# Kernel tuning notes

Measured on AMD Instinct MI355X. Metric: run time of the kernel, lower is better.

## Reference

```python
import jax, jax.numpy as jnp
import numpy as np

B, S, D, H, DFF = 2, 2048, 1024, 16, 4096
DK = D // H
EPS = 1e-5


def layer_norm(x, gamma, beta, eps=EPS):
    mu = jnp.mean(x, axis=-1, keepdims=True)
    var = jnp.mean(jnp.square(x - mu), axis=-1, keepdims=True)
    return (x - mu) * jax.lax.rsqrt(var + eps) * gamma + beta


def setup_inputs() -> dict:
    key = jax.random.key(0)
    ks = jax.random.split(key, 12)
    s_d = 1.0 / np.sqrt(D)
    s_f = 1.0 / np.sqrt(DFF)
    return {
        "x": jax.random.normal(ks[0], (B, S, D), jnp.float32),
        # per-head QKV projections stacked: [H, D, DK]
        "Wq": jax.random.normal(ks[1], (H, D, DK), jnp.float32) * s_d,
        "bq": jnp.zeros((H, DK), jnp.float32),
        "Wk": jax.random.normal(ks[2], (H, D, DK), jnp.float32) * s_d,
        "bk": jnp.zeros((H, DK), jnp.float32),
        "Wv": jax.random.normal(ks[3], (H, D, DK), jnp.float32) * s_d,
        "bv": jnp.zeros((H, DK), jnp.float32),
        "Wo": jax.random.normal(ks[4], (D, D), jnp.float32) * s_d,
        "bo": jnp.zeros((D,), jnp.float32),
        "W1": jax.random.normal(ks[5], (D, DFF), jnp.float32) * s_d,
        "b1": jnp.zeros((DFF,), jnp.float32),
        "W2": jax.random.normal(ks[6], (DFF, D), jnp.float32) * s_f,
        "b2": jnp.zeros((D,), jnp.float32),
        "ln1_g": jnp.ones((D,), jnp.float32),
        "ln1_b": jnp.zeros((D,), jnp.float32),
        "ln2_g": jnp.ones((D,), jnp.float32),
        "ln2_b": jnp.zeros((D,), jnp.float32),
    }


def reference(x, Wq, bq, Wk, bk, Wv, bv, Wo, bo, W1, b1, W2, b2,
              ln1_g, ln1_b, ln2_g, ln2_b):
    # --- residual 1: pre-norm multi-head self-attention (mask unused, dropout=eval) ---
    h = layer_norm(x, ln1_g, ln1_b)                      # [B,S,D]
    q = jnp.einsum('bsd,hdk->bhsk', h, Wq) + bq[:, None, :]
    k = jnp.einsum('bsd,hdk->bhsk', h, Wk) + bk[:, None, :]
    v = jnp.einsum('bsd,hdk->bhsk', h, Wv) + bv[:, None, :]
    scores = jnp.einsum('bhsk,bhtk->bhst', q, k) / np.sqrt(DK)  # [B,H,S,S]
    w = jax.nn.softmax(scores, axis=-1)
    ctx = jnp.einsum('bhst,bhtk->bhsk', w, v)            # [B,H,S,DK]
    # concat heads along feature dim -> [B,S,D]
    ctx = jnp.transpose(ctx, (0, 2, 1, 3)).reshape(B, S, D)
    attn_out = ctx @ Wo + bo
    x = x + attn_out
    # --- residual 2: pre-norm feed-forward ---
    h2 = layer_norm(x, ln2_g, ln2_b)
    ff = jax.nn.relu(h2 @ W1 + b1) @ W2 + b2
    return x + ff
```

## Files before the change

### kernel.cpp

```cpp
#include <hip/hip_runtime.h>

#define B_   2
#define S_   2048
#define D_   1024
#define H_   16
#define DK_  64
#define DFF_ 4096
#define NT_  (B_*S_)
#define QS_  3072

using u16 = unsigned short;
typedef __attribute__((ext_vector_type(8))) short bf16x8;
typedef __attribute__((ext_vector_type(4))) float f32x4;
typedef __attribute__((ext_vector_type(4))) u16  u16x4;

__device__ __forceinline__ float bf2f(u16 h) {
  union { unsigned u; float f; } c; c.u = ((unsigned)h) << 16; return c.f;
}
__device__ __forceinline__ u16 f2bf(float f) {
  union { float f; unsigned u; } c; c.f = f;
  unsigned u = c.u;
  return (u16)((u + 0x7fffu + ((u >> 16) & 1u)) >> 16);
}
__device__ __forceinline__ u16 f2bf_up(float f) {
  union { float f; unsigned u; } c; c.f = f;
  return (u16)((c.u + 0x8000u) >> 16);
}

__device__ __forceinline__ void load_lds16(const void* g, void* l) {
  __builtin_amdgcn_global_load_lds(
      (const __attribute__((address_space(1))) unsigned int*)g,
      (__attribute__((address_space(3))) unsigned int*)l, 16, 0, 0);
}

__device__ __forceinline__ void store_out(u16* p, float v)   { *p = f2bf(v); }
__device__ __forceinline__ void store_out(float* p, float v) { *p = v; }

__global__ __launch_bounds__(256) void ln_kernel(
    const float* __restrict__ x, const float* __restrict__ g,
    const float* __restrict__ bt, u16* __restrict__ o)
{
  const int row = blockIdx.x, t = threadIdx.x;
  const float4 xv = *(const float4*)(x + (size_t)row * D_ + t * 4);
  float f[4] = {xv.x, xv.y, xv.z, xv.w};
  float sum = f[0] + f[1] + f[2] + f[3];
  float sq  = f[0]*f[0] + f[1]*f[1] + f[2]*f[2] + f[3]*f[3];
#pragma unroll
  for (int d = 32; d >= 1; d >>= 1) {
    sum += __shfl_down(sum, d);
    sq  += __shfl_down(sq, d);
  }
  __shared__ float red[8];
  const int lane = t & 63, wid = t >> 6;
  if (lane == 0) { red[wid] = sum; red[wid + 4] = sq; }
  __syncthreads();
  sum = red[0] + red[1] + red[2] + red[3];
  sq  = red[4] + red[5] + red[6] + red[7];
  const float mu   = sum * (1.0f / D_);
  const float var  = sq * (1.0f / D_) - mu * mu;
  const float rstd = rsqrtf(var + 1e-5f);
  const float4 gv = *(const float4*)(g  + t * 4);
  const float4 bv = *(const float4*)(bt + t * 4);
  u16x4 ov;
  ov[0] = f2bf((f[0] - mu) * rstd * gv.x + bv.x);
  ov[1] = f2bf((f[1] - mu) * rstd * gv.y + bv.y);
  ov[2] = f2bf((f[2] - mu) * rstd * gv.z + bv.z);
  ov[3] = f2bf((f[3] - mu) * rstd * gv.w + bv.w);
  *(u16x4*)(o + (size_t)row * D_ + t * 4) = ov;
}

__global__ __launch_bounds__(256) void transpose_h(
    const float* __restrict__ in, u16* __restrict__ out, int R, int C)
{
  __shared__ float tile[32][33];
  const int z = blockIdx.z;
  const float* ip = in  + (size_t)z * R * C;
  u16*         op = out + (size_t)z * R * C;
  const int c0 = blockIdx.x * 32, r0 = blockIdx.y * 32;
  const int tx = threadIdx.x & 31, ty = threadIdx.x >> 5;
#pragma unroll
  for (int i = 0; i < 32; i += 8)
    tile[ty + i][tx] = ip[(size_t)(r0 + ty + i) * C + c0 + tx];
  __syncthreads();
#pragma unroll
  for (int i = 0; i < 32; i += 8)
    op[(size_t)(c0 + ty + i) * R + r0 + tx] = f2bf(tile[tx][ty + i]);
}

__global__ __launch_bounds__(256) void transpose_qkv(
    const float* __restrict__ Wq, const float* __restrict__ Wk,
    const float* __restrict__ Wv, u16* __restrict__ out)
{
  __shared__ float tile[32][33];
  const int z = blockIdx.z;
  const int which = z >> 4, h = z & 15;
  const float* ip = (which == 0 ? Wq : which == 1 ? Wk : Wv) + (size_t)h * 1024 * 64;
  u16* op = out + ((size_t)which * 1024 + h * 64) * 1024;
  const float sc = (which == 0) ? 0.125f : 1.0f;
  const int c0 = blockIdx.x * 32, r0 = blockIdx.y * 32;
  const int tx = threadIdx.x & 31, ty = threadIdx.x >> 5;
#pragma unroll
  for (int i = 0; i < 32; i += 8)
    tile[ty + i][tx] = ip[(size_t)(r0 + ty + i) * 64 + c0 + tx];
  __syncthreads();
#pragma unroll
  for (int i = 0; i < 32; i += 8)
    op[(size_t)(c0 + ty + i) * 1024 + r0 + tx] = f2bf(tile[tx][ty + i] * sc);
}

__global__ __launch_bounds__(256) void transpose_v(
    const u16* __restrict__ qkv, u16* __restrict__ vt)
{
  __shared__ u16 tile[32][33];
  const int z = blockIdx.z;
  const int b = z >> 4, h = z & 15;
  const u16* ip = qkv + (size_t)(b * S_) * QS_ + 2048 + h * DK_;
  u16* op = vt + (size_t)z * DK_ * S_;
  const int t0 = blockIdx.x * 32, d0 = blockIdx.y * 32;
  const int tx = threadIdx.x & 31, ty = threadIdx.x >> 5;
#pragma unroll
  for (int i = 0; i < 32; i += 8)
    tile[ty + i][tx] = ip[(size_t)(t0 + ty + i) * QS_ + d0 + tx];
  __syncthreads();
#pragma unroll
  for (int i = 0; i < 32; i += 8)
    op[(size_t)(d0 + ty + i) * S_ + t0 + tx] = tile[tx][ty + i];
}

template <typename OT>
__global__ __launch_bounds__(256) void gemm_bt(
    const u16* __restrict__ A, const u16* __restrict__ Bt,
    const float* __restrict__ bias, const float* __restrict__ biasB,
    const float* __restrict__ biasC, const float* __restrict__ res,
    OT* __restrict__ C, int M, int N, int K, int do_relu)
{
  __shared__ u16 lA[2][128 * 32];
  __shared__ u16 lB[2][128 * 32];
  const int tid = threadIdx.x, lane = tid & 63, wid = tid >> 6;
  const int wr = wid >> 1, wc = wid & 1;

  const int nbx = gridDim.x;
  int bid = blockIdx.y * nbx + blockIdx.x;
  const int cpx = (nbx * gridDim.y) >> 3;
  bid = (bid & 7) * cpx + (bid >> 3);
  const int row0 = (bid / nbx) * 128, col0 = (bid % nbx) * 128;

  f32x4 acc[4][4] = {};

  const int cc0 = tid, cc1 = tid + 256;
  const int r0 = cc0 >> 2, s0 = cc0 & 3;
  const int r1 = cc1 >> 2, s1 = cc1 & 3;
  const int ko0 = (s0 ^ ((r0 >> 1) & 3)) * 8;
  const int ko1 = (s1 ^ ((r1 >> 1) & 3)) * 8;

#define GST128(bf, k0)                                                        \
  {                                                                           \
    load_lds16(A  + (size_t)(row0 + r0) * K + (k0) + ko0, &lA[bf][cc0 * 8]);  \
    load_lds16(A  + (size_t)(row0 + r1) * K + (k0) + ko1, &lA[bf][cc1 * 8]);  \
    load_lds16(Bt + (size_t)(col0 + r0) * K + (k0) + ko0, &lB[bf][cc0 * 8]);  \
    load_lds16(Bt + (size_t)(col0 + r1) * K + (k0) + ko1, &lB[bf][cc1 * 8]);  \
  }

  const int nk = K >> 5;
  GST128(0, 0);
  int cur = 0;
  for (int t = 0; t < nk; ++t) {
    __syncthreads();
    if (t + 1 < nk) GST128(cur ^ 1, (t + 1) * 32);
    bf16x8 af[4], bfr[4];
#pragma unroll
    for (int m = 0; m < 4; ++m) {
      const int row = wr * 64 + m * 16 + (lane & 15);
      af[m] = *(const bf16x8*)&lA[cur][row * 32 + (((lane >> 4) ^ ((row >> 1) & 3)) * 8)];
    }
#pragma unroll
    for (int n = 0; n < 4; ++n) {
      const int row = wc * 64 + n * 16 + (lane & 15);
      bfr[n] = *(const bf16x8*)&lB[cur][row * 32 + (((lane >> 4) ^ ((row >> 1) & 3)) * 8)];
    }
#pragma unroll
    for (int m = 0; m < 4; ++m)
#pragma unroll
      for (int n = 0; n < 4; ++n)
        acc[m][n] = __builtin_amdgcn_mfma_f32_16x16x32_bf16(af[m], bfr[n], acc[m][n], 0, 0, 0);
    cur ^= 1;
  }
#undef GST128

#pragma unroll
  for (int m = 0; m < 4; ++m)
#pragma unroll
    for (int n = 0; n < 4; ++n) {
      const int rbase = row0 + wr*64 + m*16 + ((lane >> 4) << 2);
      const int c     = col0 + wc*64 + n*16 + (lane & 15);
      float bv = 0.f;
      if (biasC)      bv = c < 1024 ? bias[c] * 0.125f
                         : (c < 2048 ? biasB[c - 1024] : biasC[c - 2048]);
      else if (bias)  bv = bias[c];
#pragma unroll
      for (int r = 0; r < 4; ++r) {
        const int rr = rbase + r;
        float vv = acc[m][n][r] + bv;
        if (res) vv += res[(size_t)rr * N + c];
        if (do_relu) vv = vv > 0.f ? vv : 0.f;
        store_out(&C[(size_t)rr * N + c], vv);
      }
    }
}

template <typename OT>
__global__ __launch_bounds__(256) void gemm_bt64(
    const u16* __restrict__ A, const u16* __restrict__ Bt,
    const float* __restrict__ bias, const float* __restrict__ res,
    OT* __restrict__ C, int M, int N, int K, int do_relu)
{
  __shared__ u16 lA[2][128 * 32];
  __shared__ u16 lB[2][64 * 32];
  const int tid = threadIdx.x, lane = tid & 63, wid = tid >> 6;

  const int nbx = gridDim.x;
  int bid = blockIdx.y * nbx + blockIdx.x;
  const int cpx = (nbx * gridDim.y) >> 3;
  bid = (bid & 7) * cpx + (bid >> 3);
  const int row0 = (bid / nbx) * 128, col0 = (bid % nbx) * 64;

  f32x4 acc[2][4] = {};

  const int cc0 = tid, cc1 = tid + 256;
  const int r0 = cc0 >> 2, s0 = cc0 & 3;
  const int r1 = cc1 >> 2, s1 = cc1 & 3;
  const int ko0 = (s0 ^ ((r0 >> 1) & 3)) * 8;
  const int ko1 = (s1 ^ ((r1 >> 1) & 3)) * 8;

#define GST64(bf, k0)                                                         \
  {                                                                           \
    load_lds16(A  + (size_t)(row0 + r0) * K + (k0) + ko0, &lA[bf][cc0 * 8]);  \
    load_lds16(A  + (size_t)(row0 + r1) * K + (k0) + ko1, &lA[bf][cc1 * 8]);  \
    load_lds16(Bt + (size_t)(col0 + r0) * K + (k0) + ko0, &lB[bf][cc0 * 8]);  \
  }

  const int nk = K >> 5;
  GST64(0, 0);
  int cur = 0;
  for (int t = 0; t < nk; ++t) {
    __syncthreads();
    if (t + 1 < nk) GST64(cur ^ 1, (t + 1) * 32);
    bf16x8 af[2], bfr[4];
#pragma unroll
    for (int m = 0; m < 2; ++m) {
      const int row = wid * 32 + m * 16 + (lane & 15);
      af[m] = *(const bf16x8*)&lA[cur][row * 32 + (((lane >> 4) ^ ((row >> 1) & 3)) * 8)];
    }
#pragma unroll
    for (int n = 0; n < 4; ++n) {
      const int row = n * 16 + (lane & 15);
      bfr[n] = *(const bf16x8*)&lB[cur][row * 32 + (((lane >> 4) ^ ((row >> 1) & 3)) * 8)];
    }
#pragma unroll
    for (int m = 0; m < 2; ++m)
#pragma unroll
      for (int n = 0; n < 4; ++n)
        acc[m][n] = __builtin_amdgcn_mfma_f32_16x16x32_bf16(af[m], bfr[n], acc[m][n], 0, 0, 0);
    cur ^= 1;
  }
#undef GST64

#pragma unroll
  for (int m = 0; m < 2; ++m)
#pragma unroll
    for (int n = 0; n < 4; ++n) {
      const int rbase = row0 + wid*32 + m*16 + ((lane >> 4) << 2);
      const int c     = col0 + n*16 + (lane & 15);
      const float bv  = bias ? bias[c] : 0.f;
#pragma unroll
      for (int r = 0; r < 4; ++r) {
        const int rr = rbase + r;
        float vv = acc[m][n][r] + bv;
        if (res) vv += res[(size_t)rr * N + c];
        if (do_relu) vv = vv > 0.f ? vv : 0.f;
        store_out(&C[(size_t)rr * N + c], vv);
      }
    }
}

__global__ __launch_bounds__(256) void gemm_bt64_pk(
    const u16* __restrict__ A, const u16* __restrict__ Bt,
    float* __restrict__ P, int M, int N, int K, int KS)
{
  __shared__ u16 lA[2][128 * 32];
  __shared__ u16 lB[2][64 * 32];
  const int tid = threadIdx.x, lane = tid & 63, wid = tid >> 6;

  const int nbx = gridDim.x;
  int bid = blockIdx.y * nbx + blockIdx.x;
  const int cpx = (nbx * gridDim.y) >> 3;
  bid = (bid & 7) * cpx + (bid >> 3);
  const int row0 = (bid / nbx) * 128, col0 = (bid % nbx) * 64;
  const int kb = blockIdx.z * KS;

  f32x4 acc[2][4] = {};

  const int cc0 = tid, cc1 = tid + 256;
  const int r0 = cc0 >> 2, s0 = cc0 & 3;
  const int r1 = cc1 >> 2, s1 = cc1 & 3;
  const int ko0 = (s0 ^ ((r0 >> 1) & 3)) * 8;
  const int ko1 = (s1 ^ ((r1 >> 1) & 3)) * 8;

#define GSTPK(bf, k0)                                                              \
  {                                                                                \
    load_lds16(A  + (size_t)(row0 + r0) * K + kb + (k0) + ko0, &lA[bf][cc0 * 8]);  \
    load_lds16(A  + (size_t)(row0 + r1) * K + kb + (k0) + ko1, &lA[bf][cc1 * 8]);  \
    load_lds16(Bt + (size_t)(col0 + r0) * K + kb + (k0) + ko0, &lB[bf][cc0 * 8]);  \
  }

  const int nk = KS >> 5;
  GSTPK(0, 0);
  int cur = 0;
  for (int t = 0; t < nk; ++t) {
    __syncthreads();
    if (t + 1 < nk) GSTPK(cur ^ 1, (t + 1) * 32);
    bf16x8 af[2], bfr[4];
#pragma unroll
    for (int m = 0; m < 2; ++m) {
      const int row = wid * 32 + m * 16 + (lane & 15);
      af[m] = *(const bf16x8*)&lA[cur][row * 32 + (((lane >> 4) ^ ((row >> 1) & 3)) * 8)];
    }
#pragma unroll
    for (int n = 0; n < 4; ++n) {
      const int row = n * 16 + (lane & 15);
      bfr[n] = *(const bf16x8*)&lB[cur][row * 32 + (((lane >> 4) ^ ((row >> 1) & 3)) * 8)];
    }
#pragma unroll
    for (int m = 0; m < 2; ++m)
#pragma unroll
      for (int n = 0; n < 4; ++n)
        acc[m][n] = __builtin_amdgcn_mfma_f32_16x16x32_bf16(af[m], bfr[n], acc[m][n], 0, 0, 0);
    cur ^= 1;
  }
#undef GSTPK

  float* Pz = P + (size_t)blockIdx.z * M * N;
#pragma unroll
  for (int m = 0; m < 2; ++m)
#pragma unroll
    for (int n = 0; n < 4; ++n) {
      const int rbase = row0 + wid*32 + m*16 + ((lane >> 4) << 2);
      const int c     = col0 + n*16 + (lane & 15);
#pragma unroll
      for (int r = 0; r < 4; ++r)
        Pz[(size_t)(rbase + r) * N + c] = acc[m][n][r];
    }
}

__global__ __launch_bounds__(256) void ffr_reduce(
    const float* __restrict__ p0, const float* __restrict__ p1,
    const float* __restrict__ x1, const float* __restrict__ b2,
    float* __restrict__ out)
{
  const size_t i = (size_t)blockIdx.x * 256 + threadIdx.x;
  const float4 a  = ((const float4*)p0)[i];
  const float4 b  = ((const float4*)p1)[i];
  const float4 r  = ((const float4*)x1)[i];
  const float4 bb = ((const float4*)b2)[i & 255];
  float4 o;
  o.x = a.x + b.x + r.x + bb.x;
  o.y = a.y + b.y + r.y + bb.y;
  o.z = a.z + b.z + r.z + bb.z;
  o.w = a.w + b.w + r.w + bb.w;
  ((float4*)out)[i] = o;
}

__global__ __launch_bounds__(512) void attn_kernel(
    const u16* __restrict__ QKV, const u16* __restrict__ Vt, u16* __restrict__ O)
{
  __shared__ u16 lK[2][64 * 64];
  __shared__ u16 lV[2][64 * 64];
  __shared__ u16 lP[128 * 64];

  const int tid = threadIdx.x, lane = tid & 63, wid = tid >> 6;
  const int qt = ((blockIdx.x & 7) << 1) | (blockIdx.x >> 3);
  const int h = blockIdx.y, b = blockIdx.z;

  const u16* Qp = QKV + (size_t)(b * S_ + qt * 128) * QS_ + h * DK_;
  const u16* Kb = QKV + (size_t)(b * S_) * QS_ + 1024 + h * DK_;
  const u16* Vb = Vt  + (size_t)(b * H_ + h) * DK_ * S_;

  bf16x8 qf[2];
  {
    const int qr = wid * 16 + (lane & 15);
    qf[0] = *(const bf16x8*)(Qp + (size_t)qr * QS_ + (lane >> 4) * 8);
    qf[1] = *(const bf16x8*)(Qp + (size_t)qr * QS_ + 32 + (lane >> 4) * 8);
  }

  const bf16x8 vone = {16256,16256,16256,16256,16256,16256,16256,16256};

#define STAGE_KV(bf, kt)                                                      \
  {                                                                           \
    const u16* Kp = Kb + (size_t)(kt) * 64 * QS_;                             \
    const u16* Vp = Vb + (size_t)(kt) * 64;                                   \
    const int c = tid, r = c >> 3, sub = c & 7;                               \
    load_lds16(Kp + (size_t)r * QS_ + ((sub ^ (r & 7)) * 8), &lK[bf][c * 8]); \
    load_lds16(Vp + (size_t)r * S_  + ((sub ^ (r & 7)) * 8), &lV[bf][c * 8]); \
  }

  float m_run = -1e30f;
  f32x4 l_acc = {};
  f32x4 o_acc[4] = {};

  STAGE_KV(0, 0);
  int cur = 0;

  for (int kt = 0; kt < S_ / 64; ++kt) {
    __syncthreads();
    if (kt + 1 < S_ / 64) STAGE_KV(cur ^ 1, kt + 1);

    f32x4 s[4];
    __builtin_amdgcn_s_setprio(1);
#pragma unroll
    for (int kf = 0; kf < 4; ++kf) {
      const int row = kf * 16 + (lane & 15);
      const int i0 = (row * 64 + (lane >> 4) * 8)      ^ ((row & 7) << 3);
      const int i1 = (row * 64 + 32 + (lane >> 4) * 8) ^ ((row & 7) << 3);
      bf16x8 k0 = *(const bf16x8*)&lK[cur][i0];
      bf16x8 k1 = *(const bf16x8*)&lK[cur][i1];
      f32x4 sc = {};
      sc = __builtin_amdgcn_mfma_f32_16x16x32_bf16(k0, qf[0], sc, 0, 0, 0);
      sc = __builtin_amdgcn_mfma_f32_16x16x32_bf16(k1, qf[1], sc, 0, 0, 0);
      s[kf] = sc;
    }
    __builtin_amdgcn_s_setprio(0);

    float t0 = fmaxf(fmaxf(s[0][0], s[0][1]), fmaxf(s[0][2], s[0][3]));
    float t1 = fmaxf(fmaxf(s[1][0], s[1][1]), fmaxf(s[1][2], s[1][3]));
    float t2 = fmaxf(fmaxf(s[2][0], s[2][1]), fmaxf(s[2][2], s[2][3]));
    float t3 = fmaxf(fmaxf(s[3][0], s[3][1]), fmaxf(s[3][2], s[3][3]));
    float pmax = fmaxf(fmaxf(t0, t1), fmaxf(t2, t3));
    pmax = fmaxf(pmax, __shfl_xor(pmax, 16));
    pmax = fmaxf(pmax, __shfl_xor(pmax, 32));

    const bool grow = pmax > m_run + 8.0f;
    const float mnew = grow ? pmax : m_run;
    if (__any(grow)) {
      const float scale = __expf(m_run - mnew);
#pragma unroll
      for (int r = 0; r < 4; ++r) {
        const float sr = __shfl(scale, (lane >> 4) * 4 + r);
        l_acc[r] *= sr;
#pragma unroll
        for (int nf = 0; nf < 4; ++nf) o_acc[nf][r] *= sr;
      }
    }
    m_run = mnew;

    const int prow = wid * 16 + (lane & 15);
#pragma unroll
    for (int kf = 0; kf < 4; ++kf) {
      u16x4 pk;
#pragma unroll
      for (int r = 0; r < 4; ++r) pk[r] = f2bf_up(__expf(s[kf][r] - m_run));
      const int idx = (prow * 64 + kf * 16 + (lane >> 4) * 4) ^ ((prow & 7) << 3);
      *(u16x4*)&lP[idx] = pk;
    }
    asm volatile("s_waitcnt lgkmcnt(0)" ::: "memory");
    __builtin_amdgcn_sched_barrier(0);

    bf16x8 pa0 = *(const bf16x8*)&lP[(prow * 64 + (lane >> 4) * 8)      ^ ((prow & 7) << 3)];
    bf16x8 pa1 = *(const bf16x8*)&lP[(prow * 64 + 32 + (lane >> 4) * 8) ^ ((prow & 7) << 3)];
    __builtin_amdgcn_s_setprio(1);
    l_acc = __builtin_amdgcn_mfma_f32_16x16x32_bf16(pa0, vone, l_acc, 0, 0, 0);
    l_acc = __builtin_amdgcn_mfma_f32_16x16x32_bf16(pa1, vone, l_acc, 0, 0, 0);
#pragma unroll
    for (int nf = 0; nf < 4; ++nf) {
      const int vrow = nf * 16 + (lane & 15);
      bf16x8 v0 = *(const bf16x8*)&lV[cur][(vrow * 64 + (lane >> 4) * 8)      ^ ((vrow & 7) << 3)];
      bf16x8 v1 = *(const bf16x8*)&lV[cur][(vrow * 64 + 32 + (lane >> 4) * 8) ^ ((vrow & 7) << 3)];
      o_acc[nf] = __builtin_amdgcn_mfma_f32_16x16x32_bf16(pa0, v0, o_acc[nf], 0, 0, 0);
      o_acc[nf] = __builtin_amdgcn_mfma_f32_16x16x32_bf16(pa1, v1, o_acc[nf], 0, 0, 0);
    }
    __builtin_amdgcn_s_setprio(0);
    cur ^= 1;
  }

#pragma unroll
  for (int nf = 0; nf < 4; ++nf)
#pragma unroll
    for (int r = 0; r < 4; ++r) {
      const int qrow = qt * 128 + wid * 16 + (lane >> 4) * 4 + r;
      const int col  = h * DK_ + nf * 16 + (lane & 15);
      O[(size_t)(b * S_ + qrow) * D_ + col] = f2bf(o_acc[nf][r] / l_acc[r]);
    }
}

extern "C" void kernel_launch(void* const* d_in, const int* in_sizes, int n_in,
                              void* d_out, int out_size, void* d_ws, size_t ws_size,
                              hipStream_t stream)
{
  const float* x   = (const float*)d_in[0];
  const float* Wq  = (const float*)d_in[1];
  const float* bq  = (const float*)d_in[2];
  const float* Wk  = (const float*)d_in[3];
  const float* bk  = (const float*)d_in[4];
  const float* Wv  = (const float*)d_in[5];
  const float* bv  = (const float*)d_in[6];
  const float* Wo  = (const float*)d_in[7];
  const float* bo  = (const float*)d_in[8];
  const float* W1  = (const float*)d_in[9];
  const float* b1  = (const float*)d_in[10];
  const float* W2  = (const float*)d_in[11];
  const float* b2  = (const float*)d_in[12];
  const float* g1  = (const float*)d_in[13];
  const float* be1 = (const float*)d_in[14];
  const float* g2  = (const float*)d_in[15];
  const float* be2 = (const float*)d_in[16];
  float* out = (float*)d_out;

  const size_t MB = 1024 * 1024;
  char* base = (char*)d_ws;
  u16*   xn    = (u16*)(base);
  u16*   qkv   = (u16*)(base +  8*MB);
  u16*   ctx   = (u16*)(base + 32*MB);
  float* x1    = (float*)(base + 40*MB);
  u16*   vt    = (u16*)(base + 40*MB);
  u16*   ff1   = (u16*)(base +  8*MB);
  u16*   wqkvT = (u16*)(base + 56*MB);
  u16*   woT   = (u16*)(base + 62*MB);
  u16*   w1T   = (u16*)(base + 64*MB);
  u16*   w2T   = (u16*)(base + 72*MB);
  float* pk0   = (float*)(base + 80*MB);
  float* pk1   = (float*)(base + 96*MB);

  const bool splitk = ws_size >= (size_t)112 * MB;

  dim3 blk(256);
  transpose_qkv<<<dim3(2, 32, 48), blk, 0, stream>>>(Wq, Wk, Wv, wqkvT);
  transpose_h<<<dim3(32, 32, 1),  blk, 0, stream>>>(Wo, woT, 1024, 1024);
  transpose_h<<<dim3(128, 32, 1), blk, 0, stream>>>(W1, w1T, 1024, 4096);
  transpose_h<<<dim3(32, 128, 1), blk, 0, stream>>>(W2, w2T, 4096, 1024);

  ln_kernel<<<NT_, blk, 0, stream>>>(x, g1, be1, xn);

  gemm_bt<<<dim3(24, 32), blk, 0, stream>>>(xn, wqkvT, bq, bk, bv,
                                            (const float*)nullptr, qkv, NT_, QS_, D_, 0);

  transpose_v<<<dim3(64, 2, 32), blk, 0, stream>>>(qkv, vt);

  attn_kernel<<<dim3(S_ / 128, H_, B_), dim3(512), 0, stream>>>(qkv, vt, ctx);

  gemm_bt64<<<dim3(16, 32), blk, 0, stream>>>(ctx, woT, bo, x, x1, NT_, D_, D_, 0);

  ln_kernel<<<NT_, blk, 0, stream>>>(x1, g2, be2, xn);

  gemm_bt<<<dim3(32, 32), blk, 0, stream>>>(xn, w1T, b1, (const float*)nullptr,
                                            (const float*)nullptr, (const float*)nullptr,
                                            ff1, NT_, DFF_, D_, 1);

  if (splitk) {
    gemm_bt64_pk<<<dim3(16, 32, 2), blk, 0, stream>>>(ff1, w2T, pk0, NT_, D_, DFF_, DFF_ / 2);
    ffr_reduce<<<dim3(4096), blk, 0, stream>>>(pk0, pk1, x1, b2, out);
  } else {
    gemm_bt64<<<dim3(16, 32), blk, 0, stream>>>(ff1, w2T, b2, x1, out, NT_, D_, DFF_, 0);
  }
}
```

Baseline: 284.8 us.

## Add 256x256-tile 512-thread GEMM with 4-stage LDS pipeline for FFN1

Adds a new GEMM kernel using 256x256 output tiles, 8 waves per block, a 4-deep LDS buffer ring with prefetch three steps ahead, split half-tile MFMA phases and s_setprio around MFMA blocks. It replaces the 128-tile gemm_bt for the first FFN projection (4096x4096x1024, bias + ReLU). Larger tiles raise arithmetic intensity and cut global traffic. The cost is only 256 blocks for the device, higher register pressure from 32 accumulators, and more LDS per block.

```diff
diff --git a/kernel.cpp b/kernel.cpp
--- a/kernel.cpp
+++ b/kernel.cpp
@@ -204,6 +204,117 @@
         if (res) vv += res[(size_t)rr * N + c];
         if (do_relu) vv = vv > 0.f ? vv : 0.f;
         store_out(&C[(size_t)rr * N + c], vv);
+      }
+    }
+}
+
+template <typename OT, int KK>
+__global__ __launch_bounds__(512, 1) void gemm256(
+    const u16* __restrict__ A, const u16* __restrict__ Bt,
+    const float* __restrict__ bias, OT* __restrict__ C,
+    int M, int N, int do_relu)
+{
+  constexpr int NK = KK / 32;
+  __shared__ u16 lA[4][256 * 32];
+  __shared__ u16 lB[4][256 * 32];
+  const int tid = threadIdx.x, lane = tid & 63, wid = tid >> 6;
+  const int wr = wid >> 2, wc = wid & 3;
+
+  const int nbx = gridDim.x;
+  int bid = blockIdx.y * nbx + blockIdx.x;
+  const int cpx = (nbx * gridDim.y) >> 3;
+  bid = (bid & 7) * cpx + (bid >> 3);
+  const int row0 = (bid / nbx) * 256, col0 = (bid % nbx) * 256;
+
+  const int c0 = tid,       sr0 = c0 >> 2, q0 = ((c0 & 3) ^ (((sr0 >> 3) & 1) << 1)) * 8;
+  const int c1 = tid + 512, sr1 = c1 >> 2, q1 = ((c1 & 3) ^ (((sr1 >> 3) & 1) << 1)) * 8;
+  const u16* As0 = A  + (size_t)(row0 + sr0) * KK + q0;
+  const u16* As1 = A  + (size_t)(row0 + sr1) * KK + q1;
+  const u16* Bs0 = Bt + (size_t)(col0 + sr0) * KK + q0;
+  const u16* Bs1 = Bt + (size_t)(col0 + sr1) * KK + q1;
+
+  f32x4 acc[8][4] = {};
+  const int lrow = lane & 15, kcol = (lane >> 4) * 8;
+
+#pragma unroll
+  for (int t = 0; t < 3; ++t) {
+    load_lds16(As0 + t * 32, &lA[t][c0 * 8]);
+    load_lds16(Bs0 + t * 32, &lB[t][c0 * 8]);
+    load_lds16(As1 + t * 32, &lA[t][c1 * 8]);
+    load_lds16(Bs1 + t * 32, &lB[t][c1 * 8]);
+  }
+  asm volatile("s_waitcnt vmcnt(8)" ::: "memory");
+  __builtin_amdgcn_sched_barrier(0);
+  __builtin_amdgcn_s_barrier();
+
+#pragma unroll 4
+  for (int j = 0; j < NK; ++j) {
+    const int b = j & 3;
+    const u16* la = lA[b];
+    const u16* lb = lB[b];
+    bf16x8 af[4], bfr[4];
+
+#pragma unroll
+    for (int m = 0; m < 4; ++m) {
+      const int row = wr * 128 + m * 16 + lrow;
+      af[m] = *(const bf16x8*)&la[row * 32 + (kcol ^ (((row >> 3) & 1) << 4))];
+    }
+#pragma unroll
+    for (int n = 0; n < 4; ++n) {
+      const int row = wc * 64 + n * 16 + lrow;
+      bfr[n] = *(const bf16x8*)&lb[row * 32 + (kcol ^ (((row >> 3) & 1) << 4))];
+    }
+    if (j + 3 < NK) {
+      const int bb = (j + 3) & 3;
+      load_lds16(As0 + (j + 3) * 32, &lA[bb][c0 * 8]);
+      load_lds16(Bs0 + (j + 3) * 32, &lB[bb][c0 * 8]);
+    }
+    __builtin_amdgcn_s_setprio(1);
+#pragma unroll
+    for (int m = 0; m < 4; ++m)
+#pragma unroll
+      for (int n = 0; n < 4; ++n)
+        acc[m][n] = __builtin_amdgcn_mfma_f32_16x16x32_bf16(af[m], bfr[n], acc[m][n], 0, 0, 0);
+    __builtin_amdgcn_s_setprio(0);
+    __builtin_amdgcn_sched_barrier(0);
+    __builtin_amdgcn_s_barrier();
+
+#pragma unroll
+    for (int m = 0; m < 4; ++m) {
+      const int row = wr * 128 + (m + 4) * 16 + lrow;
+      af[m] = *(const bf16x8*)&la[row * 32 + (kcol ^ (((row >> 3) & 1) << 4))];
+    }
+    if (j + 3 < NK) {
+      const int bb = (j + 3) & 3;
+      load_lds16(As1 + (j + 3) * 32, &lA[bb][c1 * 8]);
+      load_lds16(Bs1 + (j + 3) * 32, &lB[bb][c1 * 8]);
+    }
+    __builtin_amdgcn_s_setprio(1);
+#pragma unroll
+    for (int m = 0; m < 4; ++m)
+#pragma unroll
+      for (int n = 0; n < 4; ++n)
+        acc[m + 4][n] = __builtin_amdgcn_mfma_f32_16x16x32_bf16(af[m], bfr[n], acc[m + 4][n], 0, 0, 0);
+    __builtin_amdgcn_s_setprio(0);
+    if (j + 3 < NK)      { asm volatile("s_waitcnt vmcnt(8)" ::: "memory"); }
+    else if (j + 2 < NK) { asm volatile("s_waitcnt vmcnt(4)" ::: "memory"); }
+    else if (j + 1 < NK) { asm volatile("s_waitcnt vmcnt(0)" ::: "memory"); }
+    __builtin_amdgcn_sched_barrier(0);
+    __builtin_amdgcn_s_barrier();
+  }
+
+#pragma unroll
+  for (int m = 0; m < 8; ++m)
+#pragma unroll
+    for (int n = 0; n < 4; ++n) {
+      const int rbase = row0 + wr*128 + m*16 + ((lane >> 4) << 2);
+      const int c     = col0 + wc*64 + n*16 + (lane & 15);
+      const float bv  = bias ? bias[c] : 0.f;
+#pragma unroll
+      for (int r = 0; r < 4; ++r) {
+        float vv = acc[m][n][r] + bv;
+        if (do_relu) vv = vv > 0.f ? vv : 0.f;
+        store_out(&C[(size_t)(rbase + r) * N + c], vv);
       }
     }
 }
@@ -550,9 +661,8 @@
 
   ln_kernel<<<NT_, blk, 0, stream>>>(x1, g2, be2, xn);
 
-  gemm_bt<<<dim3(32, 32), blk, 0, stream>>>(xn, w1T, b1, (const float*)nullptr,
-                                            (const float*)nullptr, (const float*)nullptr,
-                                            ff1, NT_, DFF_, D_, 1);
+  gemm256<u16, 1024><<<dim3(16, 16), dim3(512), 0, stream>>>(xn, w1T, b1, ff1,
+                                                             NT_, DFF_, 1);
 
   if (splitk) {
     gemm_bt64_pk<<<dim3(16, 32, 2), blk, 0, stream>>>(ff1, w2T, pk0, NT_, D_, DFF_, DFF_ / 2);
```

Measured after the change: 269.8 us. -5.2%, faster.
